# Kernel tuning notes

Hardware: AMD Instinct MI355X
Metric: run time of the kernel (lower is better)

Reference implementation:

```python
import jax, jax.numpy as jnp
import numpy as np

B, S, M, D, H, DH = 2, 1024, 1024, 1024, 16, 64
K = S + M                 # key length
R = 2 * K - 1             # relative position table width
EPS = 1e-5


def layer_norm(x, gamma, beta):
    mu = jnp.mean(x, axis=-1, keepdims=True)
    var = jnp.mean(jnp.square(x - mu), axis=-1, keepdims=True)
    return (x - mu) * jax.lax.rsqrt(var + EPS) * gamma + beta


def skew(q_pos, mem_len):
    # q_pos: (B, H, L, R) with R = 2*k_len - 1
    b, h, L, r = q_pos.shape
    pad = jnp.full((b, h, L, 1), -jnp.inf, q_pos.dtype)
    x = jnp.concatenate([q_pos, pad], axis=-1).reshape(b, h, L * (r + 1))
    x = x[..., : L * r].reshape(b, h, L, r)
    k_len = (r + 1) // 2
    start = k_len - 1 - mem_len
    return x[..., start : start + k_len]  # (B, H, L, k_len)


def setup_inputs() -> dict:
    key = jax.random.key(0)
    ks = jax.random.split(key, 9)
    hidden = jax.random.normal(ks[0], (B, S, D), jnp.float32)
    memory = jax.random.normal(ks[1], (B, M, D), jnp.float32)
    pos_emb = jax.random.normal(ks[2], (B, R, DH), jnp.float32)
    # causal mask: query i may attend keys j <= i + M ; True = blocked
    mask = jnp.arange(K)[None, :] > (jnp.arange(S)[:, None] + M)
    sc = 1.0 / np.sqrt(D)
    Wq = jax.random.normal(ks[3], (D, H * DH), jnp.float32) * sc
    Wk = jax.random.normal(ks[4], (D, H * DH), jnp.float32) * sc
    Wv = jax.random.normal(ks[5], (D, H * DH), jnp.float32) * sc
    Wo = jax.random.normal(ks[6], (H * DH, D), jnp.float32) * sc
    gamma = jnp.ones((D,), jnp.float32)
    beta = jnp.zeros((D,), jnp.float32)
    return {"hidden": hidden, "pos_emb": pos_emb, "memory": memory,
            "mask": mask, "Wq": Wq, "Wk": Wk, "Wv": Wv, "Wo": Wo,
            "gamma": gamma, "beta": beta}


def reference(hidden, pos_emb, memory, mask, Wq, Wk, Wv, Wo, gamma, beta):
    mem_len = memory.shape[1]
    combined = jnp.concatenate([memory, hidden], axis=1)  # (B, K, D)
    h_ln = layer_norm(hidden, gamma, beta)                # pre-LN
    c_ln = layer_norm(combined, gamma, beta)
    q = (h_ln @ Wq).reshape(B, S, H, DH).transpose(0, 2, 1, 3)  # (B,H,S,DH)
    k = (c_ln @ Wk).reshape(B, K, H, DH).transpose(0, 2, 1, 3)  # (B,H,K,DH)
    v = (c_ln @ Wv).reshape(B, K, H, DH).transpose(0, 2, 1, 3)
    score = jnp.einsum('bhsd,bhkd->bhsk', q, k)                  # (B,H,S,K)
    q_pos = jnp.einsum('bhsd,brd->bhsr', q, pos_emb)             # (B,H,S,R)
    score = (score + skew(q_pos, mem_len)) * (1.0 / np.sqrt(D))
    score = jnp.where(mask[None, None], -jnp.inf, score)
    p = jax.nn.softmax(score, axis=-1)
    attn = jnp.einsum('bhsk,bhkd->bshd', p, v).reshape(B, S, H * DH)
    out = attn @ Wo
    return h_ln + out
```

## Files before the change

kernel.cpp:

```cpp
#include <hip/hip_runtime.h>
#include <hip/hip_bf16.h>

#define B_ 2
#define S_ 1024
#define M_ 1024
#define D_ 1024
#define H_ 16
#define DH_ 64
#define K_ 2048
#define R_ 4095

#define NEG_BIG (-1e30f)

typedef unsigned short u16;
typedef short short8 __attribute__((ext_vector_type(8)));
typedef float f32x4 __attribute__((ext_vector_type(4)));

__device__ __forceinline__ u16 f2bf(float f) {
  __hip_bfloat16 h = __float2bfloat16(f);
  return *reinterpret_cast<u16*>(&h);
}
__device__ __forceinline__ float bf2f(u16 u) {
  __hip_bfloat16 h;
  *reinterpret_cast<u16*>(&h) = u;
  return __bfloat162float(h);
}

__device__ __forceinline__ void gll16(const void* g, const void* l) {
  __builtin_amdgcn_global_load_lds(
      (const __attribute__((address_space(1))) unsigned int*)g,
      (__attribute__((address_space(3))) unsigned int*)l, 16, 0, 0);
}

__device__ __forceinline__ f32x4 mfma16(short8 a, short8 b, f32x4 c) {
  return __builtin_amdgcn_mfma_f32_16x16x32_bf16(a, b, c, 0, 0, 0);
}

__global__ __launch_bounds__(256) void prep_kernel(
    const float* __restrict__ hidden, const float* __restrict__ memory,
    const float* __restrict__ gamma, const float* __restrict__ beta,
    u16* __restrict__ cln,
    const float* __restrict__ W0, const float* __restrict__ W1,
    const float* __restrict__ W2, const float* __restrict__ W3,
    u16* __restrict__ O0, u16* __restrict__ O1,
    u16* __restrict__ O2, u16* __restrict__ O3,
    const float* __restrict__ pos, u16* __restrict__ posT) {
  __shared__ u16 tile[64][66];
  __shared__ float red[8];
  const int bx = blockIdx.x;
  const int t = threadIdx.x;

  if (bx < 4096) {
    const int b = bx >> 11;
    const int idx = bx & (K_ - 1);
    const float* src = (idx < M_)
        ? memory + (size_t)(b * M_ + idx) * D_
        : hidden + (size_t)(b * S_ + (idx - M_)) * D_;
    const int lane = t & 63, w = t >> 6;
    float4 rv = ((const float4*)src)[t];
    float s = rv.x + rv.y + rv.z + rv.w;
    float ss = rv.x * rv.x + rv.y * rv.y + rv.z * rv.z + rv.w * rv.w;
#pragma unroll
    for (int m = 1; m < 64; m <<= 1) {
      s += __shfl_xor(s, m, 64);
      ss += __shfl_xor(ss, m, 64);
    }
    if (lane == 0) { red[w] = s; red[4 + w] = ss; }
    __syncthreads();
    s = red[0] + red[1] + red[2] + red[3];
    ss = red[4] + red[5] + red[6] + red[7];
    const float mu = s * (1.0f / D_);
    const float var = ss * (1.0f / D_) - mu * mu;
    const float rstd = rsqrtf(var + 1e-5f);
    float4 gv = ((const float4*)gamma)[t];
    float4 bv = ((const float4*)beta)[t];
    ushort4 ov;
    ov.x = f2bf((rv.x - mu) * rstd * gv.x + bv.x);
    ov.y = f2bf((rv.y - mu) * rstd * gv.y + bv.y);
    ov.z = f2bf((rv.z - mu) * rstd * gv.z + bv.z);
    ov.w = f2bf((rv.w - mu) * rstd * gv.w + bv.w);
    ((ushort4*)(cln + (size_t)bx * D_))[t] = ov;
    return;
  }
  if (bx < 5120) {
    const int z = (bx - 4096) >> 8;
    const int rem = (bx - 4096) & 255;
    const float* in; u16* out;
    switch (z) {
      case 0:  in = W0; out = O0; break;
      case 1:  in = W1; out = O1; break;
      case 2:  in = W2; out = O2; break;
      default: in = W3; out = O3; break;
    }
    const int tx = t & 63, ty = t >> 6;
    const int k0 = (rem & 15) * 64, n0 = (rem >> 4) * 64;
#pragma unroll
    for (int i = ty; i < 64; i += 4)
      tile[i][tx] = f2bf(in[(size_t)(k0 + i) * D_ + n0 + tx]);
    __syncthreads();
#pragma unroll
    for (int i = ty; i < 64; i += 4)
      out[(size_t)(n0 + i) * D_ + k0 + tx] = tile[tx][i];
    return;
  }
  {
    const int u = (bx - 5120) * 256 + t;
    const int oct = u & 7;
    const int r = (u >> 3) & 15;
    const int g = (u >> 7) % 136;
    const int b = u / 17408;
    const int row = g * 16 + r;
    const float* s = pos + ((size_t)b * R_ + row) * 64 + oct * 8;
    float4 v0 = ((const float4*)s)[0];
    float4 v1 = ((const float4*)s)[1];
    ushort4 oA, oB;
    oA.x = f2bf(v0.x); oA.y = f2bf(v0.y); oA.z = f2bf(v0.z); oA.w = f2bf(v0.w);
    oB.x = f2bf(v1.x); oB.y = f2bf(v1.y); oB.z = f2bf(v1.z); oB.w = f2bf(v1.w);
    u16* d = posT + (size_t)(b * 136 + g) * 1024 + oct * 128 + r * 8;
    ((ushort4*)d)[0] = oA;
    ((ushort4*)d)[1] = oB;
  }
}

__device__ __forceinline__ int maprow_hidden(int r) {
  return r + ((r >> 10) << 10) + M_;
}

__global__ __launch_bounds__(256, 3) void gemm_qkv_kernel(
    const u16* __restrict__ A, const u16* __restrict__ Bt,
    u16* __restrict__ qb, u16* __restrict__ kb, u16* __restrict__ vbT) {
  __shared__ __align__(16) u16 As[128 * 64];
  __shared__ __align__(16) u16 Bs[128 * 64];
  const int t = threadIdx.x;
  const int lane = t & 63, w = t >> 6;
  const int wm = w >> 1, wn = w & 1;
  const int qd = lane >> 4, lr = lane & 15;
  const int m0 = blockIdx.y * 128, n0 = blockIdx.x * 128;
  if (n0 < 1024 && !(m0 & 1024)) return;

  const int swz = ((t & 7) ^ ((t >> 3) & 7)) * 8;
  const int c0 = (qd ^ (lr & 7)) * 8;
  const int c1 = c0 ^ 32;
  const int row8 = (t >> 3) & 7;

  f32x4 acc[4][4];
#pragma unroll
  for (int mt = 0; mt < 4; mt++)
#pragma unroll
    for (int nt = 0; nt < 4; nt++) acc[mt][nt] = (f32x4){0.f, 0.f, 0.f, 0.f};

  for (int kt = 0; kt < 1024; kt += 64) {
#pragma unroll
    for (int p = 0; p < 4; p++) {
      const int ra = w * 32 + p * 8 + row8;
      gll16(A + (size_t)(m0 + ra) * 1024 + kt + swz, As + (w * 32 + p * 8) * 64);
      gll16(Bt + (size_t)(n0 + ra) * 1024 + kt + swz, Bs + (w * 32 + p * 8) * 64);
    }
    __syncthreads();
    short8 a0[4], a1[4], b0[4], b1[4];
#pragma unroll
    for (int mt = 0; mt < 4; mt++) {
      a0[mt] = *(const short8*)&As[(wm * 64 + mt * 16 + lr) * 64 + c0];
      a1[mt] = *(const short8*)&As[(wm * 64 + mt * 16 + lr) * 64 + c1];
    }
#pragma unroll
    for (int nt = 0; nt < 4; nt++) {
      b0[nt] = *(const short8*)&Bs[(wn * 64 + nt * 16 + lr) * 64 + c0];
      b1[nt] = *(const short8*)&Bs[(wn * 64 + nt * 16 + lr) * 64 + c1];
    }
#pragma unroll
    for (int mt = 0; mt < 4; mt++)
#pragma unroll
      for (int nt = 0; nt < 4; nt++) {
        acc[mt][nt] = mfma16(a0[mt], b0[nt], acc[mt][nt]);
        acc[mt][nt] = mfma16(a1[mt], b1[nt], acc[mt][nt]);
      }
    __syncthreads();
  }

#pragma unroll
  for (int mt = 0; mt < 4; mt++)
#pragma unroll
    for (int nt = 0; nt < 4; nt++) {
      const int colb = n0 + wn * 64 + nt * 16;
      const int rowb = m0 + wm * 64 + mt * 16 + qd * 4;
      if (colb < 1024) {
        const int qrow = ((rowb >> 11) << 10) | (rowb & 1023);
#pragma unroll
        for (int r = 0; r < 4; r++)
          qb[(size_t)(qrow + r) * 1024 + colb + lr] = f2bf(acc[mt][nt][r] * 0.03125f);
      } else if (colb < 2048) {
        const int key = rowb & (K_ - 1);
        const int bq = rowb >> 11;
#pragma unroll
        for (int r = 0; r < 4; r++)
          kb[(size_t)(bq * K_ + key + r) * 1024 + (colb - 1024) + lr] = f2bf(acc[mt][nt][r]);
      } else {
        const int nn = colb - 2048 + lr;
        const int bh = ((rowb >> 11) << 4) | (nn >> 6);
        const int dh = nn & 63;
        const int key = rowb & (K_ - 1);
        ushort4 pk;
        pk.x = f2bf(acc[mt][nt][0]);
        pk.y = f2bf(acc[mt][nt][1]);
        pk.z = f2bf(acc[mt][nt][2]);
        pk.w = f2bf(acc[mt][nt][3]);
        *(ushort4*)&vbT[((size_t)bh * 64 + dh) * K_ + key] = pk;
      }
    }
}

__global__ __launch_bounds__(256, 2) void out_gemm_kernel(
    const u16* __restrict__ A, const u16* __restrict__ Bt,
    const u16* __restrict__ resid, float* __restrict__ Cf) {
  __shared__ __align__(16) u16 As[128 * 32];
  __shared__ __align__(16) u16 Bs[64 * 32];
  const int t = threadIdx.x;
  const int lane = t & 63, w = t >> 6;
  const int wm = w >> 1, wn = w & 1;
  const int qd = lane >> 4, lr = lane & 15;
  const int m0 = blockIdx.y * 128, n0 = blockIdx.x * 64;

  const u16* Ag0 = A + (size_t)(m0 + (t >> 2)) * 1024 + (t & 3) * 8;
  const u16* Ag1 = Ag0 + (size_t)64 * 1024;
  const u16* Bg0 = Bt + (size_t)(n0 + (t >> 2)) * 1024 + (t & 3) * 8;

  f32x4 acc[4][2];
#pragma unroll
  for (int mt = 0; mt < 4; mt++)
#pragma unroll
    for (int nt = 0; nt < 2; nt++) acc[mt][nt] = (f32x4){0.f, 0.f, 0.f, 0.f};

  for (int kt = 0; kt < 1024; kt += 32) {
    gll16(Ag0 + kt, As + w * 512);
    gll16(Ag1 + kt, As + 2048 + w * 512);
    gll16(Bg0 + kt, Bs + w * 512);
    __syncthreads();
    short8 af[4], bfr[2];
#pragma unroll
    for (int mt = 0; mt < 4; mt++)
      af[mt] = *(const short8*)&As[(wm * 64 + mt * 16 + lr) * 32 + qd * 8];
#pragma unroll
    for (int nt = 0; nt < 2; nt++)
      bfr[nt] = *(const short8*)&Bs[(wn * 32 + nt * 16 + lr) * 32 + qd * 8];
#pragma unroll
    for (int mt = 0; mt < 4; mt++)
#pragma unroll
      for (int nt = 0; nt < 2; nt++)
        acc[mt][nt] = mfma16(af[mt], bfr[nt], acc[mt][nt]);
    __syncthreads();
  }

#pragma unroll
  for (int mt = 0; mt < 4; mt++)
#pragma unroll
    for (int nt = 0; nt < 2; nt++)
#pragma unroll
      for (int r = 0; r < 4; r++) {
        const int row = m0 + wm * 64 + mt * 16 + qd * 4 + r;
        const int col = n0 + wn * 32 + nt * 16 + lr;
        float v = acc[mt][nt][r] + bf2f(resid[(size_t)maprow_hidden(row) * 1024 + col]);
        Cf[(size_t)row * 1024 + col] = v;
      }
}

__global__ __launch_bounds__(256, 2) void attn_kernel(
    const u16* __restrict__ qb, const u16* __restrict__ kb,
    const u16* __restrict__ vbT, const u16* __restrict__ posT,
    u16* __restrict__ ab) {
  __shared__ __align__(16) u16 Ks[2][64 * 64];
  __shared__ __align__(16) u16 Vt[2][64 * 64];
  __shared__ __align__(16) u16 Pt[4][16 * 64];

  const int t = threadIdx.x;
  const int lane = t & 63, w = t >> 6;
  const int qd = lane >> 4, lr = lane & 15;

  const int flat = blockIdx.x + 16 * blockIdx.y + 256 * blockIdx.z;
  const int xcd = flat & 7;
  const int slot = flat >> 3;
  const int gsub = slot >> 4;
  int qt = slot & 15;
  if (gsub & 2) qt = 15 - qt;
  const int g = gsub * 8 + xcd;
  const int h = g & 15;
  const int b = g >> 4;
  const int i0 = qt * 64;

  const int swz = ((t & 7) ^ ((t >> 3) & 7)) * 8;
  const int c0 = (qd ^ (lr & 7)) * 8;
  const int c1 = c0 ^ 32;
  const int row8 = t >> 3;

  const int jmax = min(K_, i0 + 64 + M_);

  const int g0 = 63 - (i0 >> 4) - w;
  const u16* pb0 = posT + (size_t)b * 139264 + qd * 128 + lr * 8;

#pragma unroll
  for (int rd = 0; rd < 2; rd++)
    gll16(qb + (size_t)(b * S_ + i0 + rd * 32 + row8) * 1024 + h * 64 + swz,
          &Ks[1][0] + rd * 2048 + w * 512);
#pragma unroll
  for (int rd = 0; rd < 2; rd++) {
    gll16(kb + (size_t)(b * K_ + rd * 32 + row8) * 1024 + h * 64 + swz,
          &Ks[0][0] + rd * 2048 + w * 512);
    gll16(vbT + (size_t)((b * H_ + h) * 64 + rd * 32 + row8) * K_ + swz,
          &Vt[0][0] + rd * 2048 + w * 512);
  }
  short8 pg0[5], pg1[5];
  {
    const u16* pp = pb0 + (size_t)g0 * 1024;
#pragma unroll
    for (int pc = 0; pc < 5; pc++) {
      pg0[pc] = *(const short8*)(pp + pc * 1024);
      pg1[pc] = *(const short8*)(pp + pc * 1024 + 512);
    }
  }
  __syncthreads();
  const short8 aQ0 = *(const short8*)&Ks[1][(w * 16 + lr) * 64 + c0];
  const short8 aQ1 = *(const short8*)&Ks[1][(w * 16 + lr) * 64 + c1];

  f32x4 accO[4];
#pragma unroll
  for (int d = 0; d < 4; d++) accO[d] = (f32x4){0.f, 0.f, 0.f, 0.f};
  float lsum[4];
#pragma unroll
  for (int r = 0; r < 4; r++) lsum[r] = 0.f;

  int cur = 0;

  for (int j0 = 0, tt = 0; j0 < jmax; j0 += 64, tt++) {
    __syncthreads();
    if (j0 + 64 < jmax) {
      const int nxt = cur ^ 1;
#pragma unroll
      for (int rd = 0; rd < 2; rd++) {
        gll16(kb + (size_t)(b * K_ + j0 + 64 + rd * 32 + row8) * 1024 + h * 64 + swz,
              &Ks[nxt][0] + rd * 2048 + w * 512);
        gll16(vbT + (size_t)((b * H_ + h) * 64 + rd * 32 + row8) * K_ + j0 + 64 + swz,
              &Vt[nxt][0] + rd * 2048 + w * 512);
      }
    }

    f32x4 zp[5];
#pragma unroll
    for (int pc = 0; pc < 5; pc++) {
      f32x4 z = {0.f, 0.f, 0.f, 0.f};
      z = mfma16(aQ0, pg0[pc], z);
      zp[pc] = mfma16(aQ1, pg1[pc], z);
    }

    f32x4 sqk[4];
#pragma unroll
    for (int kc = 0; kc < 4; kc++) {
      const short8 bK0 = *(const short8*)&Ks[cur][(kc * 16 + lr) * 64 + c0];
      const short8 bK1 = *(const short8*)&Ks[cur][(kc * 16 + lr) * 64 + c1];
      f32x4 z = {0.f, 0.f, 0.f, 0.f};
      z = mfma16(aQ0, bK0, z);
      sqk[kc] = mfma16(aQ1, bK1, z);
    }

    {
      const u16* pn = pb0 + (size_t)(g0 + 4 * (tt + 1)) * 1024;
#pragma unroll
      for (int pc = 0; pc < 5; pc++) {
        pg0[pc] = *(const short8*)(pn + pc * 1024);
        pg1[pc] = *(const short8*)(pn + pc * 1024 + 512);
      }
    }

    const bool tail = (j0 + 63 > i0 + w * 16 + M_);
    float p[4][4];
#pragma unroll
    for (int r = 0; r < 4; r++) {
      const int iL = qd * 4 + r;
      const int d = 15 + lr - iL;
      const int srcl = qd * 16 + (d & 15);
      const bool hi = (d >> 4) & 1;
      float g0s = __shfl(zp[0][r], srcl, 64);
      float g1s = __shfl(zp[1][r], srcl, 64);
      float g2s = __shfl(zp[2][r], srcl, 64);
      float g3s = __shfl(zp[3][r], srcl, 64);
      float g4s = __shfl(zp[4][r], srcl, 64);
      float s0 = sqk[0][r] + (hi ? g1s : g0s);
      float s1 = sqk[1][r] + (hi ? g2s : g1s);
      float s2 = sqk[2][r] + (hi ? g3s : g2s);
      float s3 = sqk[3][r] + (hi ? g4s : g3s);
      if (tail) {
        const int key = j0 + lr, lim = i0 + w * 16 + iL + M_;
        if (key      > lim) s0 = NEG_BIG;
        if (key + 16 > lim) s1 = NEG_BIG;
        if (key + 32 > lim) s2 = NEG_BIG;
        if (key + 48 > lim) s3 = NEG_BIG;
      }
      p[0][r] = __expf(s0);
      p[1][r] = __expf(s1);
      p[2][r] = __expf(s2);
      p[3][r] = __expf(s3);
      lsum[r] += p[0][r] + p[1][r] + p[2][r] + p[3][r];
    }

#pragma unroll
    for (int r = 0; r < 4; r++) {
      const int row = qd * 4 + r;
      const int cbase = row * 64;
      const int rx = row & 7;
      const int lo = lr & 7, hi8 = lr >> 3;
#pragma unroll
      for (int kc = 0; kc < 4; kc++)
        Pt[w][cbase + ((((kc << 1) | hi8) ^ rx) << 3) + lo] = f2bf(p[kc][r]);
    }
    __asm__ volatile("s_waitcnt lgkmcnt(0)" ::: "memory");
    const short8 aP0 = *(const short8*)&Pt[w][lr * 64 + ((qd ^ (lr & 7)) << 3)];
    const short8 aP1 = *(const short8*)&Pt[w][lr * 64 + (((qd + 4) ^ (lr & 7)) << 3)];

#pragma unroll
    for (int d2 = 0; d2 < 4; d2++) {
      const short8 bV0 = *(const short8*)&Vt[cur][(d2 * 16 + lr) * 64 + c0];
      const short8 bV1 = *(const short8*)&Vt[cur][(d2 * 16 + lr) * 64 + c1];
      accO[d2] = mfma16(aP0, bV0, accO[d2]);
      accO[d2] = mfma16(aP1, bV1, accO[d2]);
    }

    cur ^= 1;
  }

  float inv[4];
#pragma unroll
  for (int r = 0; r < 4; r++) {
#pragma unroll
    for (int msk = 1; msk < 16; msk <<= 1) lsum[r] += __shfl_xor(lsum[r], msk, 64);
    inv[r] = 1.0f / lsum[r];
  }
#pragma unroll
  for (int d2 = 0; d2 < 4; d2++)
#pragma unroll
    for (int r = 0; r < 4; r++) {
      const int iG = i0 + w * 16 + qd * 4 + r;
      ab[(size_t)(b * S_ + iG) * 1024 + h * 64 + d2 * 16 + lr] = f2bf(accO[d2][r] * inv[r]);
    }
}

extern "C" void kernel_launch(void* const* d_in, const int* in_sizes, int n_in,
                              void* d_out, int out_size, void* d_ws, size_t ws_size,
                              hipStream_t stream) {
  const float* hidden = (const float*)d_in[0];
  const float* pos    = (const float*)d_in[1];
  const float* memory = (const float*)d_in[2];
  const float* Wq = (const float*)d_in[4];
  const float* Wk = (const float*)d_in[5];
  const float* Wv = (const float*)d_in[6];
  const float* Wo = (const float*)d_in[7];
  const float* gamma = (const float*)d_in[8];
  const float* beta  = (const float*)d_in[9];

  char* ws = (char*)d_ws;
  u16* cln  = (u16*)(ws);
  u16* qb   = (u16*)(ws + 8388608);
  u16* kb   = (u16*)(ws + 12582912);
  u16* vbT  = (u16*)(ws + 20971520);
  u16* ab   = (u16*)(ws + 29360128);
  u16* WqT  = (u16*)(ws + 33554432);
  u16* WkT  = WqT + 1048576;
  u16* WvT  = WkT + 1048576;
  u16* WoT  = WvT + 1048576;
  u16* posT = (u16*)(ws + 41943040);

  prep_kernel<<<dim3(5256), 256, 0, stream>>>(
      hidden, memory, gamma, beta, cln,
      Wq, Wk, Wv, Wo, WqT, WkT, WvT, WoT, pos, posT);
  gemm_qkv_kernel<<<dim3(24, 32), 256, 0, stream>>>(cln, WqT, qb, kb, vbT);
  attn_kernel<<<dim3(S_ / 64, H_, B_), 256, 0, stream>>>(qb, kb, vbT, posT, ab);
  out_gemm_kernel<<<dim3(16, 16), 256, 0, stream>>>(ab, WoT, cln, (float*)d_out);
}
```

Measured before the change: 207.0 us.

## Software-pipeline PV matmul one tile behind QK with triple-buffered V tiles

Defers each tile's P·V MFMA work to the next iteration, issuing it right after the QK MFMAs so matrix work overlaps the softmax/exp phase. V tiles move to a three-slot ring so the previous tile's V stays resident while the next is prefetched, and a final epilogue drains the last deferred tile. It also raises wave priority around the MFMA block via s_setprio. The cost is extra LDS (one more 8KB V buffer), which may reduce occupancy under launch_bounds(256,2), plus extra live registers for the carried P fragments.

```diff
diff --git a/kernel.cpp b/kernel.cpp
--- a/kernel.cpp
+++ b/kernel.cpp
@@ -269,7 +269,7 @@
     const u16* __restrict__ vbT, const u16* __restrict__ posT,
     u16* __restrict__ ab) {
   __shared__ __align__(16) u16 Ks[2][64 * 64];
-  __shared__ __align__(16) u16 Vt[2][64 * 64];
+  __shared__ __align__(16) u16 Vt[3][64 * 64];
   __shared__ __align__(16) u16 Pt[4][16 * 64];
 
   const int t = threadIdx.x;
@@ -328,21 +328,24 @@
 #pragma unroll
   for (int r = 0; r < 4; r++) lsum[r] = 0.f;
 
-  int cur = 0;
+  short8 aPp0 = {}, aPp1 = {};
+  int vprev = 0, vcur = 0;
 
   for (int j0 = 0, tt = 0; j0 < jmax; j0 += 64, tt++) {
     __syncthreads();
+    const int vnxt = (vcur == 2) ? 0 : vcur + 1;
     if (j0 + 64 < jmax) {
-      const int nxt = cur ^ 1;
+      const int knxt = (tt + 1) & 1;
 #pragma unroll
       for (int rd = 0; rd < 2; rd++) {
         gll16(kb + (size_t)(b * K_ + j0 + 64 + rd * 32 + row8) * 1024 + h * 64 + swz,
-              &Ks[nxt][0] + rd * 2048 + w * 512);
+              &Ks[knxt][0] + rd * 2048 + w * 512);
         gll16(vbT + (size_t)((b * H_ + h) * 64 + rd * 32 + row8) * K_ + j0 + 64 + swz,
-              &Vt[nxt][0] + rd * 2048 + w * 512);
-      }
-    }
-
+              &Vt[vnxt][0] + rd * 2048 + w * 512);
+      }
+    }
+
+    __builtin_amdgcn_s_setprio(1);
     f32x4 zp[5];
 #pragma unroll
     for (int pc = 0; pc < 5; pc++) {
@@ -354,12 +357,23 @@
     f32x4 sqk[4];
 #pragma unroll
     for (int kc = 0; kc < 4; kc++) {
-      const short8 bK0 = *(const short8*)&Ks[cur][(kc * 16 + lr) * 64 + c0];
-      const short8 bK1 = *(const short8*)&Ks[cur][(kc * 16 + lr) * 64 + c1];
+      const short8 bK0 = *(const short8*)&Ks[tt & 1][(kc * 16 + lr) * 64 + c0];
+      const short8 bK1 = *(const short8*)&Ks[tt & 1][(kc * 16 + lr) * 64 + c1];
       f32x4 z = {0.f, 0.f, 0.f, 0.f};
       z = mfma16(aQ0, bK0, z);
       sqk[kc] = mfma16(aQ1, bK1, z);
     }
+
+    if (tt > 0) {
+#pragma unroll
+      for (int d2 = 0; d2 < 4; d2++) {
+        const short8 bV0 = *(const short8*)&Vt[vprev][(d2 * 16 + lr) * 64 + c0];
+        const short8 bV1 = *(const short8*)&Vt[vprev][(d2 * 16 + lr) * 64 + c1];
+        accO[d2] = mfma16(aPp0, bV0, accO[d2]);
+        accO[d2] = mfma16(aPp1, bV1, accO[d2]);
+      }
+    }
+    __builtin_amdgcn_s_setprio(0);
 
     {
       const u16* pn = pb0 + (size_t)(g0 + 4 * (tt + 1)) * 1024;
@@ -412,18 +426,19 @@
         Pt[w][cbase + ((((kc << 1) | hi8) ^ rx) << 3) + lo] = f2bf(p[kc][r]);
     }
     __asm__ volatile("s_waitcnt lgkmcnt(0)" ::: "memory");
-    const short8 aP0 = *(const short8*)&Pt[w][lr * 64 + ((qd ^ (lr & 7)) << 3)];
-    const short8 aP1 = *(const short8*)&Pt[w][lr * 64 + (((qd + 4) ^ (lr & 7)) << 3)];
-
-#pragma unroll
-    for (int d2 = 0; d2 < 4; d2++) {
-      const short8 bV0 = *(const short8*)&Vt[cur][(d2 * 16 + lr) * 64 + c0];
-      const short8 bV1 = *(const short8*)&Vt[cur][(d2 * 16 + lr) * 64 + c1];
-      accO[d2] = mfma16(aP0, bV0, accO[d2]);
-      accO[d2] = mfma16(aP1, bV1, accO[d2]);
-    }
-
-    cur ^= 1;
+    aPp0 = *(const short8*)&Pt[w][lr * 64 + ((qd ^ (lr & 7)) << 3)];
+    aPp1 = *(const short8*)&Pt[w][lr * 64 + (((qd + 4) ^ (lr & 7)) << 3)];
+
+    vprev = vcur;
+    vcur = vnxt;
+  }
+
+#pragma unroll
+  for (int d2 = 0; d2 < 4; d2++) {
+    const short8 bV0 = *(const short8*)&Vt[vprev][(d2 * 16 + lr) * 64 + c0];
+    const short8 bV1 = *(const short8*)&Vt[vprev][(d2 * 16 + lr) * 64 + c1];
+    accO[d2] = mfma16(aPp0, bV0, accO[d2]);
+    accO[d2] = mfma16(aPp1, bV1, accO[d2]);
   }
 
   float inv[4];
```

Measured after the change: 205.4 us. About the same (-0.8%).

## Process two 64-key tiles per barrier in attention loop with MFMA priority hints

Applied to the files above, without the earlier changes.

The attention kernel's key loop now handles 128 keys per iteration as two 64-key sub-tiles. K/V shared buffers are doubled so both next sub-tiles are prefetched together, and the positional-embedding fragments for both sub-tiles are held in registers. This halves the number of __syncthreads per key span. s_setprio raises wave priority around the MFMA sections. The posT per-batch stride grows from 136 to 144 groups, presumably so the extra-ahead positional prefetch stays in bounds. Shared memory use doubles (about 40KB per block) and register pressure rises, which may reduce occupancy below the two blocks per CU the launch bounds request.

```diff
diff --git a/kernel.cpp b/kernel.cpp
--- a/kernel.cpp
+++ b/kernel.cpp
@@ -116,7 +116,7 @@
     ushort4 oA, oB;
     oA.x = f2bf(v0.x); oA.y = f2bf(v0.y); oA.z = f2bf(v0.z); oA.w = f2bf(v0.w);
     oB.x = f2bf(v1.x); oB.y = f2bf(v1.y); oB.z = f2bf(v1.z); oB.w = f2bf(v1.w);
-    u16* d = posT + (size_t)(b * 136 + g) * 1024 + oct * 128 + r * 8;
+    u16* d = posT + (size_t)(b * 144 + g) * 1024 + oct * 128 + r * 8;
     ((ushort4*)d)[0] = oA;
     ((ushort4*)d)[1] = oB;
   }
@@ -268,8 +268,8 @@
     const u16* __restrict__ qb, const u16* __restrict__ kb,
     const u16* __restrict__ vbT, const u16* __restrict__ posT,
     u16* __restrict__ ab) {
-  __shared__ __align__(16) u16 Ks[2][64 * 64];
-  __shared__ __align__(16) u16 Vt[2][64 * 64];
+  __shared__ __align__(16) u16 Ks[2][2][64 * 64];
+  __shared__ __align__(16) u16 Vt[2][2][64 * 64];
   __shared__ __align__(16) u16 Pt[4][16 * 64];
 
   const int t = threadIdx.x;
@@ -295,31 +295,39 @@
   const int jmax = min(K_, i0 + 64 + M_);
 
   const int g0 = 63 - (i0 >> 4) - w;
-  const u16* pb0 = posT + (size_t)b * 139264 + qd * 128 + lr * 8;
+  const u16* pb0 = posT + (size_t)b * 147456 + qd * 128 + lr * 8;
 
 #pragma unroll
   for (int rd = 0; rd < 2; rd++)
     gll16(qb + (size_t)(b * S_ + i0 + rd * 32 + row8) * 1024 + h * 64 + swz,
-          &Ks[1][0] + rd * 2048 + w * 512);
-#pragma unroll
-  for (int rd = 0; rd < 2; rd++) {
-    gll16(kb + (size_t)(b * K_ + rd * 32 + row8) * 1024 + h * 64 + swz,
-          &Ks[0][0] + rd * 2048 + w * 512);
-    gll16(vbT + (size_t)((b * H_ + h) * 64 + rd * 32 + row8) * K_ + swz,
-          &Vt[0][0] + rd * 2048 + w * 512);
-  }
-  short8 pg0[5], pg1[5];
+          &Ks[1][0][0] + rd * 2048 + w * 512);
+#pragma unroll
+  for (int sb = 0; sb < 2; sb++)
+#pragma unroll
+    for (int rd = 0; rd < 2; rd++) {
+      gll16(kb + (size_t)(b * K_ + sb * 64 + rd * 32 + row8) * 1024 + h * 64 + swz,
+            &Ks[0][sb][0] + rd * 2048 + w * 512);
+      gll16(vbT + (size_t)((b * H_ + h) * 64 + rd * 32 + row8) * K_ + sb * 64 + swz,
+            &Vt[0][sb][0] + rd * 2048 + w * 512);
+    }
+  short8 pgA0[5], pgA1[5], pgB0[5], pgB1[5];
   {
     const u16* pp = pb0 + (size_t)g0 * 1024;
 #pragma unroll
     for (int pc = 0; pc < 5; pc++) {
-      pg0[pc] = *(const short8*)(pp + pc * 1024);
-      pg1[pc] = *(const short8*)(pp + pc * 1024 + 512);
+      pgA0[pc] = *(const short8*)(pp + pc * 1024);
+      pgA1[pc] = *(const short8*)(pp + pc * 1024 + 512);
+    }
+    const u16* p2 = pb0 + (size_t)(g0 + 4) * 1024;
+#pragma unroll
+    for (int pc = 0; pc < 5; pc++) {
+      pgB0[pc] = *(const short8*)(p2 + pc * 1024);
+      pgB1[pc] = *(const short8*)(p2 + pc * 1024 + 512);
     }
   }
   __syncthreads();
-  const short8 aQ0 = *(const short8*)&Ks[1][(w * 16 + lr) * 64 + c0];
-  const short8 aQ1 = *(const short8*)&Ks[1][(w * 16 + lr) * 64 + c1];
+  const short8 aQ0 = *(const short8*)&Ks[1][0][(w * 16 + lr) * 64 + c0];
+  const short8 aQ1 = *(const short8*)&Ks[1][0][(w * 16 + lr) * 64 + c1];
 
   f32x4 accO[4];
 #pragma unroll
@@ -328,102 +336,185 @@
 #pragma unroll
   for (int r = 0; r < 4; r++) lsum[r] = 0.f;
 
-  int cur = 0;
-
-  for (int j0 = 0, tt = 0; j0 < jmax; j0 += 64, tt++) {
-    __syncthreads();
+  for (int j0 = 0, ph = 0; j0 < jmax; j0 += 128, ph++) {
+    __syncthreads();
+    const int cb = ph & 1;
+    const int nb = cb ^ 1;
+    const int j0n = j0 + 128;
+#pragma unroll
+    for (int sb = 0; sb < 2; sb++)
+      if (j0n + sb * 64 < jmax) {
+#pragma unroll
+        for (int rd = 0; rd < 2; rd++) {
+          gll16(kb + (size_t)(b * K_ + j0n + sb * 64 + rd * 32 + row8) * 1024 + h * 64 + swz,
+                &Ks[nb][sb][0] + rd * 2048 + w * 512);
+          gll16(vbT + (size_t)((b * H_ + h) * 64 + rd * 32 + row8) * K_ + j0n + sb * 64 + swz,
+                &Vt[nb][sb][0] + rd * 2048 + w * 512);
+        }
+      }
+
+    {
+      __builtin_amdgcn_s_setprio(1);
+      f32x4 zp[5];
+#pragma unroll
+      for (int pc = 0; pc < 5; pc++) {
+        f32x4 z = {0.f, 0.f, 0.f, 0.f};
+        z = mfma16(aQ0, pgA0[pc], z);
+        zp[pc] = mfma16(aQ1, pgA1[pc], z);
+      }
+      f32x4 sqk[4];
+#pragma unroll
+      for (int kc = 0; kc < 4; kc++) {
+        const short8 bK0 = *(const short8*)&Ks[cb][0][(kc * 16 + lr) * 64 + c0];
+        const short8 bK1 = *(const short8*)&Ks[cb][0][(kc * 16 + lr) * 64 + c1];
+        f32x4 z = {0.f, 0.f, 0.f, 0.f};
+        z = mfma16(aQ0, bK0, z);
+        sqk[kc] = mfma16(aQ1, bK1, z);
+      }
+      __builtin_amdgcn_s_setprio(0);
+      {
+        const u16* pn = pb0 + (size_t)(g0 + 4 * (2 * ph + 2)) * 1024;
+#pragma unroll
+        for (int pc = 0; pc < 5; pc++) {
+          pgA0[pc] = *(const short8*)(pn + pc * 1024);
+          pgA1[pc] = *(const short8*)(pn + pc * 1024 + 512);
+        }
+      }
+      const bool tail = (j0 + 63 > i0 + w * 16 + M_);
+      float p[4][4];
+#pragma unroll
+      for (int r = 0; r < 4; r++) {
+        const int iL = qd * 4 + r;
+        const int d = 15 + lr - iL;
+        const int srcl = qd * 16 + (d & 15);
+        const bool hi = (d >> 4) & 1;
+        float g0s = __shfl(zp[0][r], srcl, 64);
+        float g1s = __shfl(zp[1][r], srcl, 64);
+        float g2s = __shfl(zp[2][r], srcl, 64);
+        float g3s = __shfl(zp[3][r], srcl, 64);
+        float g4s = __shfl(zp[4][r], srcl, 64);
+        float s0 = sqk[0][r] + (hi ? g1s : g0s);
+        float s1 = sqk[1][r] + (hi ? g2s : g1s);
+        float s2 = sqk[2][r] + (hi ? g3s : g2s);
+        float s3 = sqk[3][r] + (hi ? g4s : g3s);
+        if (tail) {
+          const int key = j0 + lr, lim = i0 + w * 16 + iL + M_;
+          if (key      > lim) s0 = NEG_BIG;
+          if (key + 16 > lim) s1 = NEG_BIG;
+          if (key + 32 > lim) s2 = NEG_BIG;
+          if (key + 48 > lim) s3 = NEG_BIG;
+        }
+        p[0][r] = __expf(s0);
+        p[1][r] = __expf(s1);
+        p[2][r] = __expf(s2);
+        p[3][r] = __expf(s3);
+        lsum[r] += p[0][r] + p[1][r] + p[2][r] + p[3][r];
+      }
+#pragma unroll
+      for (int r = 0; r < 4; r++) {
+        const int row = qd * 4 + r;
+        const int cbase = row * 64;
+        const int rx = row & 7;
+        const int lo = lr & 7, hi8 = lr >> 3;
+#pragma unroll
+        for (int kc = 0; kc < 4; kc++)
+          Pt[w][cbase + ((((kc << 1) | hi8) ^ rx) << 3) + lo] = f2bf(p[kc][r]);
+      }
+      __asm__ volatile("s_waitcnt lgkmcnt(0)" ::: "memory");
+      const short8 aP0 = *(const short8*)&Pt[w][lr * 64 + ((qd ^ (lr & 7)) << 3)];
+      const short8 aP1 = *(const short8*)&Pt[w][lr * 64 + (((qd + 4) ^ (lr & 7)) << 3)];
+      __builtin_amdgcn_s_setprio(1);
+#pragma unroll
+      for (int d2 = 0; d2 < 4; d2++) {
+        const short8 bV0 = *(const short8*)&Vt[cb][0][(d2 * 16 + lr) * 64 + c0];
+        const short8 bV1 = *(const short8*)&Vt[cb][0][(d2 * 16 + lr) * 64 + c1];
+        accO[d2] = mfma16(aP0, bV0, accO[d2]);
+        accO[d2] = mfma16(aP1, bV1, accO[d2]);
+      }
+      __builtin_amdgcn_s_setprio(0);
+    }
+
     if (j0 + 64 < jmax) {
-      const int nxt = cur ^ 1;
-#pragma unroll
-      for (int rd = 0; rd < 2; rd++) {
-        gll16(kb + (size_t)(b * K_ + j0 + 64 + rd * 32 + row8) * 1024 + h * 64 + swz,
-              &Ks[nxt][0] + rd * 2048 + w * 512);
-        gll16(vbT + (size_t)((b * H_ + h) * 64 + rd * 32 + row8) * K_ + j0 + 64 + swz,
-              &Vt[nxt][0] + rd * 2048 + w * 512);
-      }
-    }
-
-    f32x4 zp[5];
-#pragma unroll
-    for (int pc = 0; pc < 5; pc++) {
-      f32x4 z = {0.f, 0.f, 0.f, 0.f};
-      z = mfma16(aQ0, pg0[pc], z);
-      zp[pc] = mfma16(aQ1, pg1[pc], z);
-    }
-
-    f32x4 sqk[4];
-#pragma unroll
-    for (int kc = 0; kc < 4; kc++) {
-      const short8 bK0 = *(const short8*)&Ks[cur][(kc * 16 + lr) * 64 + c0];
-      const short8 bK1 = *(const short8*)&Ks[cur][(kc * 16 + lr) * 64 + c1];
-      f32x4 z = {0.f, 0.f, 0.f, 0.f};
-      z = mfma16(aQ0, bK0, z);
-      sqk[kc] = mfma16(aQ1, bK1, z);
-    }
-
-    {
-      const u16* pn = pb0 + (size_t)(g0 + 4 * (tt + 1)) * 1024;
+      const int j1 = j0 + 64;
+      __builtin_amdgcn_s_setprio(1);
+      f32x4 zp[5];
 #pragma unroll
       for (int pc = 0; pc < 5; pc++) {
-        pg0[pc] = *(const short8*)(pn + pc * 1024);
-        pg1[pc] = *(const short8*)(pn + pc * 1024 + 512);
-      }
-    }
-
-    const bool tail = (j0 + 63 > i0 + w * 16 + M_);
-    float p[4][4];
-#pragma unroll
-    for (int r = 0; r < 4; r++) {
-      const int iL = qd * 4 + r;
-      const int d = 15 + lr - iL;
-      const int srcl = qd * 16 + (d & 15);
-      const bool hi = (d >> 4) & 1;
-      float g0s = __shfl(zp[0][r], srcl, 64);
-      float g1s = __shfl(zp[1][r], srcl, 64);
-      float g2s = __shfl(zp[2][r], srcl, 64);
-      float g3s = __shfl(zp[3][r], srcl, 64);
-      float g4s = __shfl(zp[4][r], srcl, 64);
-      float s0 = sqk[0][r] + (hi ? g1s : g0s);
-      float s1 = sqk[1][r] + (hi ? g2s : g1s);
-      float s2 = sqk[2][r] + (hi ? g3s : g2s);
-      float s3 = sqk[3][r] + (hi ? g4s : g3s);
-      if (tail) {
-        const int key = j0 + lr, lim = i0 + w * 16 + iL + M_;
-        if (key      > lim) s0 = NEG_BIG;
-        if (key + 16 > lim) s1 = NEG_BIG;
-        if (key + 32 > lim) s2 = NEG_BIG;
-        if (key + 48 > lim) s3 = NEG_BIG;
-      }
-      p[0][r] = __expf(s0);
-      p[1][r] = __expf(s1);
-      p[2][r] = __expf(s2);
-      p[3][r] = __expf(s3);
-      lsum[r] += p[0][r] + p[1][r] + p[2][r] + p[3][r];
-    }
-
-#pragma unroll
-    for (int r = 0; r < 4; r++) {
-      const int row = qd * 4 + r;
-      const int cbase = row * 64;
-      const int rx = row & 7;
-      const int lo = lr & 7, hi8 = lr >> 3;
-#pragma unroll
-      for (int kc = 0; kc < 4; kc++)
-        Pt[w][cbase + ((((kc << 1) | hi8) ^ rx) << 3) + lo] = f2bf(p[kc][r]);
-    }
-    __asm__ volatile("s_waitcnt lgkmcnt(0)" ::: "memory");
-    const short8 aP0 = *(const short8*)&Pt[w][lr * 64 + ((qd ^ (lr & 7)) << 3)];
-    const short8 aP1 = *(const short8*)&Pt[w][lr * 64 + (((qd + 4) ^ (lr & 7)) << 3)];
-
-#pragma unroll
-    for (int d2 = 0; d2 < 4; d2++) {
-      const short8 bV0 = *(const short8*)&Vt[cur][(d2 * 16 + lr) * 64 + c0];
-      const short8 bV1 = *(const short8*)&Vt[cur][(d2 * 16 + lr) * 64 + c1];
-      accO[d2] = mfma16(aP0, bV0, accO[d2]);
-      accO[d2] = mfma16(aP1, bV1, accO[d2]);
-    }
-
-    cur ^= 1;
+        f32x4 z = {0.f, 0.f, 0.f, 0.f};
+        z = mfma16(aQ0, pgB0[pc], z);
+        zp[pc] = mfma16(aQ1, pgB1[pc], z);
+      }
+      f32x4 sqk[4];
+#pragma unroll
+      for (int kc = 0; kc < 4; kc++) {
+        const short8 bK0 = *(const short8*)&Ks[cb][1][(kc * 16 + lr) * 64 + c0];
+        const short8 bK1 = *(const short8*)&Ks[cb][1][(kc * 16 + lr) * 64 + c1];
+        f32x4 z = {0.f, 0.f, 0.f, 0.f};
+        z = mfma16(aQ0, bK0, z);
+        sqk[kc] = mfma16(aQ1, bK1, z);
+      }
+      __builtin_amdgcn_s_setprio(0);
+      {
+        const u16* pn = pb0 + (size_t)(g0 + 4 * (2 * ph + 3)) * 1024;
+#pragma unroll
+        for (int pc = 0; pc < 5; pc++) {
+          pgB0[pc] = *(const short8*)(pn + pc * 1024);
+          pgB1[pc] = *(const short8*)(pn + pc * 1024 + 512);
+        }
+      }
+      const bool tail = (j1 + 63 > i0 + w * 16 + M_);
+      float p[4][4];
+#pragma unroll
+      for (int r = 0; r < 4; r++) {
+        const int iL = qd * 4 + r;
+        const int d = 15 + lr - iL;
+        const int srcl = qd * 16 + (d & 15);
+        const bool hi = (d >> 4) & 1;
+        float g0s = __shfl(zp[0][r], srcl, 64);
+        float g1s = __shfl(zp[1][r], srcl, 64);
+        float g2s = __shfl(zp[2][r], srcl, 64);
+        float g3s = __shfl(zp[3][r], srcl, 64);
+        float g4s = __shfl(zp[4][r], srcl, 64);
+        float s0 = sqk[0][r] + (hi ? g1s : g0s);
+        float s1 = sqk[1][r] + (hi ? g2s : g1s);
+        float s2 = sqk[2][r] + (hi ? g3s : g2s);
+        float s3 = sqk[3][r] + (hi ? g4s : g3s);
+        if (tail) {
+          const int key = j1 + lr, lim = i0 + w * 16 + iL + M_;
+          if (key      > lim) s0 = NEG_BIG;
+          if (key + 16 > lim) s1 = NEG_BIG;
+          if (key + 32 > lim) s2 = NEG_BIG;
+          if (key + 48 > lim) s3 = NEG_BIG;
+        }
+        p[0][r] = __expf(s0);
+        p[1][r] = __expf(s1);
+        p[2][r] = __expf(s2);
+        p[3][r] = __expf(s3);
+        lsum[r] += p[0][r] + p[1][r] + p[2][r] + p[3][r];
+      }
+#pragma unroll
+      for (int r = 0; r < 4; r++) {
+        const int row = qd * 4 + r;
+        const int cbase = row * 64;
+        const int rx = row & 7;
+        const int lo = lr & 7, hi8 = lr >> 3;
+#pragma unroll
+        for (int kc = 0; kc < 4; kc++)
+          Pt[w][cbase + ((((kc << 1) | hi8) ^ rx) << 3) + lo] = f2bf(p[kc][r]);
+      }
+      __asm__ volatile("s_waitcnt lgkmcnt(0)" ::: "memory");
+      const short8 aP0 = *(const short8*)&Pt[w][lr * 64 + ((qd ^ (lr & 7)) << 3)];
+      const short8 aP1 = *(const short8*)&Pt[w][lr * 64 + (((qd + 4) ^ (lr & 7)) << 3)];
+      __builtin_amdgcn_s_setprio(1);
+#pragma unroll
+      for (int d2 = 0; d2 < 4; d2++) {
+        const short8 bV0 = *(const short8*)&Vt[cb][1][(d2 * 16 + lr) * 64 + c0];
+        const short8 bV1 = *(const short8*)&Vt[cb][1][(d2 * 16 + lr) * 64 + c1];
+        accO[d2] = mfma16(aP0, bV0, accO[d2]);
+        accO[d2] = mfma16(aP1, bV1, accO[d2]);
+      }
+      __builtin_amdgcn_s_setprio(0);
+    }
   }
 
   float inv[4];
```

Result: faster. 202.4 us (-2.2%).
